# Performance work log

Measured on AMD Instinct MI355X. Metric: run time of the kernel, lower is better.

The kernel has to match this reference:

```python
import jax, jax.numpy as jnp
import numpy as np

U, H, R, N = 128, 5120, 160, 32  # users, d_inner, dt_rank, d_state(padded)


def setup_inputs() -> dict:
    key = jax.random.key(0)
    ks = jax.random.split(key, 8)
    s_in = 1.0 / np.sqrt(H)
    s_r = 1.0 / np.sqrt(R)
    x = jax.random.normal(ks[0], (1, 1, U, H), dtype=jnp.float32)
    h_prev = jnp.zeros((U, H, N), dtype=jnp.float32)
    W_dt_low = jax.random.normal(ks[1], (H, R), dtype=jnp.float32) * s_in
    W_dt = jax.random.normal(ks[2], (R, H), dtype=jnp.float32) * s_r
    b_dt = jax.random.normal(ks[3], (H,), dtype=jnp.float32) * 0.1
    W_B = jax.random.normal(ks[4], (H, N), dtype=jnp.float32) * s_in
    W_C = jax.random.normal(ks[5], (H, N), dtype=jnp.float32) * s_in
    # A = -exp(A_log): strictly negative, as in Mamba preprocessing
    A = -jnp.exp(jax.random.normal(ks[6], (H, N), dtype=jnp.float32) * 0.5)
    D = jax.random.normal(ks[7], (H,), dtype=jnp.float32)
    return {"x": x, "h_prev": h_prev, "W_dt_low": W_dt_low, "W_dt": W_dt,
            "b_dt": b_dt, "W_B": W_B, "W_C": W_C, "A": A, "D": D}


def reference(x, h_prev, W_dt_low, W_dt, b_dt, W_B, W_C, A, D):
    xf = x[0, 0]                                        # (U, H)
    # delta: low-rank projection then dt_proj + bias, softplus (beta=1, thresh=20)
    z = (xf @ W_dt_low) @ W_dt + b_dt                    # (U, H)
    delta = jnp.where(z > 20.0, z, jax.nn.softplus(z))   # (U, H)
    B = xf @ W_B                                         # (U, N)
    C = xf @ W_C                                         # (U, N)
    # discretized recurrence: h' = exp(delta*A)*h + delta*B*x
    abar = jnp.exp(delta[:, :, None] * A[None])          # (U, H, N)
    h_new = abar * h_prev + delta[:, :, None] * B[:, None, :] * xf[:, :, None]
    y = jnp.einsum('uhn,un->uh', h_new, C)               # (U, H)
    out = xf * D[None, :] + y                            # (U, H)
    return out[None, None]                               # (1, 1, U, H)
```

## Files before the change

### kernel.cpp

```cpp
#include <hip/hip_runtime.h>

#define UU 128
#define HH 5120
#define RR 160
#define NS 32

__global__ __launch_bounds__(320) void k1_dtlow(const float* __restrict__ x,
                                                const float* __restrict__ Wdl,
                                                float* __restrict__ dtlP) {
    const int ut = blockIdx.x >> 4;
    const int hc = blockIdx.x & 15;
    const int u0 = ut * 8;
    const int h0 = hc * 320;
    const int t  = threadIdx.x;
    __shared__ __attribute__((aligned(16))) float xs[320 * 8];
    #pragma unroll
    for (int i = 0; i < 8; ++i)
        xs[t * 8 + i] = x[(u0 + i) * HH + h0 + t];
    __syncthreads();
    const int r    = t % 160;
    const int half = t / 160;
    float a0 = 0.f, a1 = 0.f, a2 = 0.f, a3 = 0.f;
    const float* wp = Wdl + (size_t)h0 * RR + r;
    #pragma unroll 4
    for (int hh = 0; hh < 320; ++hh) {
        float w = wp[hh * RR];
        float4 xv = *(const float4*)&xs[hh * 8 + half * 4];
        a0 += xv.x * w; a1 += xv.y * w; a2 += xv.z * w; a3 += xv.w * w;
    }
    float* o = dtlP + hc * (UU * RR) + (u0 + half * 4) * RR + r;
    o[0] = a0; o[RR] = a1; o[2 * RR] = a2; o[3 * RR] = a3;
}

__global__ __launch_bounds__(256) void k2b_bc(const float* __restrict__ x,
                                              const float* __restrict__ WB,
                                              const float* __restrict__ WC,
                                              float* __restrict__ bcP) {
    const int ut = blockIdx.x >> 3;
    const int hc = blockIdx.x & 7;
    const int u0 = ut * 8;
    const int h0 = hc * 640;
    const int t  = threadIdx.x;
    __shared__ __attribute__((aligned(16))) float xs[640 * 8];
    for (int i = t; i < 640 * 8; i += 256) {
        int hh = i % 640, ul = i / 640;
        xs[hh * 8 + ul] = x[(u0 + ul) * HH + h0 + hh];
    }
    __syncthreads();
    const int col = t & 63, n = col & 31, mat = (col >> 5) & 1, hq = t >> 6;
    const float* W = (mat ? WC : WB) + (size_t)(h0 + hq * 160) * NS + n;
    float acc[8] = {0.f, 0.f, 0.f, 0.f, 0.f, 0.f, 0.f, 0.f};
    #pragma unroll 4
    for (int hh = 0; hh < 160; ++hh) {
        float w = W[hh * NS];
        const float* xp = &xs[(hq * 160 + hh) * 8];
        float4 a = *(const float4*)xp;
        float4 b = *(const float4*)(xp + 4);
        acc[0] += a.x * w; acc[1] += a.y * w; acc[2] += a.z * w; acc[3] += a.w * w;
        acc[4] += b.x * w; acc[5] += b.y * w; acc[6] += b.z * w; acc[7] += b.w * w;
    }
    __syncthreads();
    #pragma unroll
    for (int ul = 0; ul < 8; ++ul) xs[t * 8 + ul] = acc[ul];
    __syncthreads();
    if (hq == 0) {
        #pragma unroll
        for (int ul = 0; ul < 8; ++ul) {
            float s = xs[t * 8 + ul] + xs[(t + 64) * 8 + ul]
                    + xs[(t + 128) * 8 + ul] + xs[(t + 192) * 8 + ul];
            bcP[hc * (UU * 64) + (u0 + ul) * 64 + col] = s;
        }
    }
}

__global__ __launch_bounds__(256) void k2_delta(const float* __restrict__ dtlP,
                                                const float* __restrict__ Wdt,
                                                const float* __restrict__ bdt,
                                                const float* __restrict__ bcP,
                                                float* __restrict__ BC,
                                                float* __restrict__ delta) {
    const int ut = blockIdx.x / 20;
    const int ht = blockIdx.x % 20;
    const int u0 = ut * 8, h0 = ht * 256, t = threadIdx.x;
    __shared__ __attribute__((aligned(16))) float dtl[RR * 8];
    for (int i = t; i < RR * 8; i += 256) {
        int r = i % RR, ul = i / RR;
        float s = 0.f;
        #pragma unroll
        for (int hc = 0; hc < 16; ++hc)
            s += dtlP[hc * (UU * RR) + (u0 + ul) * RR + r];
        dtl[r * 8 + ul] = s;
    }
    if (ht == 0) {
        for (int i = t; i < 512; i += 256) {
            int ul = i >> 6, col = i & 63;
            float s = 0.f;
            #pragma unroll
            for (int hc = 0; hc < 8; ++hc)
                s += bcP[hc * (UU * 64) + (u0 + ul) * 64 + col];
            BC[(u0 + ul) * 64 + col] = s;
        }
    }
    __syncthreads();
    const int h = h0 + t;
    float acc[8] = {0.f, 0.f, 0.f, 0.f, 0.f, 0.f, 0.f, 0.f};
    #pragma unroll 4
    for (int r = 0; r < RR; ++r) {
        float w = Wdt[(size_t)r * HH + h];
        float4 a = *(const float4*)&dtl[r * 8];
        float4 b = *(const float4*)&dtl[r * 8 + 4];
        acc[0] += a.x * w; acc[1] += a.y * w; acc[2] += a.z * w; acc[3] += a.w * w;
        acc[4] += b.x * w; acc[5] += b.y * w; acc[6] += b.z * w; acc[7] += b.w * w;
    }
    const float bv = bdt[h];
    #pragma unroll
    for (int ul = 0; ul < 8; ++ul) {
        float z = acc[ul] + bv;
        float d = (z > 20.f) ? z : __logf(1.f + __expf(z));
        delta[(size_t)(u0 + ul) * HH + h] = d;
    }
}

__global__ __launch_bounds__(256) void k3_main(const float* __restrict__ x,
                                               const float* __restrict__ hprev,
                                               const float* __restrict__ A,
                                               const float* __restrict__ Dp,
                                               const float* __restrict__ BC,
                                               const float* __restrict__ delta,
                                               float* __restrict__ out) {
    const int u  = blockIdx.x / 160;
    const int ht = blockIdx.x % 160;
    const int t  = threadIdx.x;
    __shared__ __attribute__((aligned(16))) float bc[64];
    if (t < 64) bc[t] = BC[u * 64 + t];
    __syncthreads();
    const int g = t >> 3;
    const int l = t & 7;
    const int h = ht * 32 + g;
    const float d  = delta[(size_t)u * HH + h];
    const float xv = x[(size_t)u * HH + h];
    const float4 a4 = *(const float4*)&A[(size_t)h * NS + l * 4];
    const float4 hp = *(const float4*)&hprev[((size_t)u * HH + h) * NS + l * 4];
    const float4 b4 = *(const float4*)&bc[l * 4];
    const float4 c4 = *(const float4*)&bc[32 + l * 4];
    const float dx = d * xv;
    float4 hn;
    hn.x = __expf(d * a4.x) * hp.x + dx * b4.x;
    hn.y = __expf(d * a4.y) * hp.y + dx * b4.y;
    hn.z = __expf(d * a4.z) * hp.z + dx * b4.z;
    hn.w = __expf(d * a4.w) * hp.w + dx * b4.w;
    float y = hn.x * c4.x + hn.y * c4.y + hn.z * c4.z + hn.w * c4.w;
    y += __shfl_xor(y, 1);
    y += __shfl_xor(y, 2);
    y += __shfl_xor(y, 4);
    if (l == 0) out[(size_t)u * HH + h] = xv * Dp[h] + y;
}

extern "C" void kernel_launch(void* const* d_in, const int* in_sizes, int n_in,
                              void* d_out, int out_size, void* d_ws, size_t ws_size,
                              hipStream_t stream) {
    const float* x     = (const float*)d_in[0];
    const float* hprev = (const float*)d_in[1];
    const float* Wdl   = (const float*)d_in[2];
    const float* Wdt   = (const float*)d_in[3];
    const float* bdt   = (const float*)d_in[4];
    const float* WB    = (const float*)d_in[5];
    const float* WC    = (const float*)d_in[6];
    const float* A     = (const float*)d_in[7];
    const float* Dp    = (const float*)d_in[8];
    float* out = (float*)d_out;
    float* ws  = (float*)d_ws;

    float* dtlP  = ws;
    float* bcP   = ws + 327680;
    float* BC    = ws + 393216;
    float* delta = ws + 401408;

    k1_dtlow<<<256, 320, 0, stream>>>(x, Wdl, dtlP);
    k2b_bc  <<<128, 256, 0, stream>>>(x, WB, WC, bcP);
    k2_delta<<<320, 256, 0, stream>>>(dtlP, Wdt, bdt, bcP, BC, delta);
    k3_main <<<20480, 256, 0, stream>>>(x, hprev, A, Dp, BC, delta, out);
}
```

Baseline: 227.0 us.

## Fuse dt-low and B/C projections into one kernel; one thread per channel in main

Merges the low-rank dt projection and the B/C projections into a single kernel with 32 h-chunks, and transposes the partial-sum layout to [col][u] so results can be written as float4. The delta kernel now reduces over 32 partials instead of 16 and 8. The main kernel switches from 8 lanes per channel with shuffle reduction to one thread per channel looping over all 32 states, cutting the block count from 20480 to 2560. Risks include uncoalesced per-thread 128-byte hprev reads in the main kernel, 32 idle threads per block in the projection kernel, and more partial sums to reduce.

```diff
diff --git a/kernel.cpp b/kernel.cpp
--- a/kernel.cpp
+++ b/kernel.cpp
@@ -5,75 +5,56 @@
 #define RR 160
 #define NS 32
 
-__global__ __launch_bounds__(320) void k1_dtlow(const float* __restrict__ x,
-                                                const float* __restrict__ Wdl,
-                                                float* __restrict__ dtlP) {
-    const int ut = blockIdx.x >> 4;
-    const int hc = blockIdx.x & 15;
+__global__ __launch_bounds__(256) void ka_proj(const float* __restrict__ x,
+                                               const float* __restrict__ Wdl,
+                                               const float* __restrict__ WB,
+                                               const float* __restrict__ WC,
+                                               float* __restrict__ dtlP,
+                                               float* __restrict__ bcP) {
+    const int ut = blockIdx.x >> 5;
+    const int hc = blockIdx.x & 31;
     const int u0 = ut * 8;
-    const int h0 = hc * 320;
+    const int h0 = hc * 160;
     const int t  = threadIdx.x;
-    __shared__ __attribute__((aligned(16))) float xs[320 * 8];
+    __shared__ __attribute__((aligned(16))) float xs[160 * 8];
     #pragma unroll
-    for (int i = 0; i < 8; ++i)
-        xs[t * 8 + i] = x[(u0 + i) * HH + h0 + t];
-    __syncthreads();
-    const int r    = t % 160;
-    const int half = t / 160;
-    float a0 = 0.f, a1 = 0.f, a2 = 0.f, a3 = 0.f;
-    const float* wp = Wdl + (size_t)h0 * RR + r;
-    #pragma unroll 4
-    for (int hh = 0; hh < 320; ++hh) {
-        float w = wp[hh * RR];
-        float4 xv = *(const float4*)&xs[hh * 8 + half * 4];
-        a0 += xv.x * w; a1 += xv.y * w; a2 += xv.z * w; a3 += xv.w * w;
-    }
-    float* o = dtlP + hc * (UU * RR) + (u0 + half * 4) * RR + r;
-    o[0] = a0; o[RR] = a1; o[2 * RR] = a2; o[3 * RR] = a3;
-}
-
-__global__ __launch_bounds__(256) void k2b_bc(const float* __restrict__ x,
-                                              const float* __restrict__ WB,
-                                              const float* __restrict__ WC,
-                                              float* __restrict__ bcP) {
-    const int ut = blockIdx.x >> 3;
-    const int hc = blockIdx.x & 7;
-    const int u0 = ut * 8;
-    const int h0 = hc * 640;
-    const int t  = threadIdx.x;
-    __shared__ __attribute__((aligned(16))) float xs[640 * 8];
-    for (int i = t; i < 640 * 8; i += 256) {
-        int hh = i % 640, ul = i / 640;
+    for (int k = 0; k < 5; ++k) {
+        int i  = t + k * 256;
+        int ul = i / 160, hh = i % 160;
         xs[hh * 8 + ul] = x[(u0 + ul) * HH + h0 + hh];
     }
     __syncthreads();
-    const int col = t & 63, n = col & 31, mat = (col >> 5) & 1, hq = t >> 6;
-    const float* W = (mat ? WC : WB) + (size_t)(h0 + hq * 160) * NS + n;
-    float acc[8] = {0.f, 0.f, 0.f, 0.f, 0.f, 0.f, 0.f, 0.f};
+    const int c = t;
+    const float* wp;
+    int stride;
+    float* outp = nullptr;
+    if (c < 160) {
+        wp = Wdl + (size_t)h0 * RR + c;          stride = RR;
+        outp = dtlP + hc * (RR * UU) + c * UU + u0;
+    } else if (c < 224) {
+        int col = c - 160;
+        wp = ((col < 32) ? WB : WC) + (size_t)h0 * NS + (col & 31);
+        stride = NS;
+        outp = bcP + hc * (64 * UU) + col * UU + u0;
+    } else {
+        wp = Wdl; stride = 0;
+    }
+    float a[8] = {0.f, 0.f, 0.f, 0.f, 0.f, 0.f, 0.f, 0.f};
     #pragma unroll 4
     for (int hh = 0; hh < 160; ++hh) {
-        float w = W[hh * NS];
-        const float* xp = &xs[(hq * 160 + hh) * 8];
-        float4 a = *(const float4*)xp;
-        float4 b = *(const float4*)(xp + 4);
-        acc[0] += a.x * w; acc[1] += a.y * w; acc[2] += a.z * w; acc[3] += a.w * w;
-        acc[4] += b.x * w; acc[5] += b.y * w; acc[6] += b.z * w; acc[7] += b.w * w;
+        float w = wp[hh * stride];
+        float4 x0 = *(const float4*)&xs[hh * 8];
+        float4 x1 = *(const float4*)&xs[hh * 8 + 4];
+        a[0] += x0.x * w; a[1] += x0.y * w; a[2] += x0.z * w; a[3] += x0.w * w;
+        a[4] += x1.x * w; a[5] += x1.y * w; a[6] += x1.z * w; a[7] += x1.w * w;
     }
-    __syncthreads();
-    #pragma unroll
-    for (int ul = 0; ul < 8; ++ul) xs[t * 8 + ul] = acc[ul];
-    __syncthreads();
-    if (hq == 0) {
-        #pragma unroll
-        for (int ul = 0; ul < 8; ++ul) {
-            float s = xs[t * 8 + ul] + xs[(t + 64) * 8 + ul]
-                    + xs[(t + 128) * 8 + ul] + xs[(t + 192) * 8 + ul];
-            bcP[hc * (UU * 64) + (u0 + ul) * 64 + col] = s;
-        }
+    if (outp) {
+        *(float4*)&outp[0] = make_float4(a[0], a[1], a[2], a[3]);
+        *(float4*)&outp[4] = make_float4(a[4], a[5], a[6], a[7]);
     }
 }
 
-__global__ __launch_bounds__(256) void k2_delta(const float* __restrict__ dtlP,
+__global__ __launch_bounds__(256) void kb_delta(const float* __restrict__ dtlP,
                                                 const float* __restrict__ Wdt,
                                                 const float* __restrict__ bdt,
                                                 const float* __restrict__ bcP,
@@ -83,21 +64,25 @@
     const int ht = blockIdx.x % 20;
     const int u0 = ut * 8, h0 = ht * 256, t = threadIdx.x;
     __shared__ __attribute__((aligned(16))) float dtl[RR * 8];
-    for (int i = t; i < RR * 8; i += 256) {
-        int r = i % RR, ul = i / RR;
+    #pragma unroll
+    for (int k = 0; k < 5; ++k) {
+        int i = t + k * 256;
+        int r = i >> 3, ul = i & 7;
         float s = 0.f;
         #pragma unroll
-        for (int hc = 0; hc < 16; ++hc)
-            s += dtlP[hc * (UU * RR) + (u0 + ul) * RR + r];
-        dtl[r * 8 + ul] = s;
+        for (int hc = 0; hc < 32; ++hc)
+            s += dtlP[hc * (RR * UU) + r * UU + u0 + ul];
+        dtl[i] = s;
     }
     if (ht == 0) {
-        for (int i = t; i < 512; i += 256) {
+        #pragma unroll
+        for (int k = 0; k < 2; ++k) {
+            int i = t + k * 256;
             int ul = i >> 6, col = i & 63;
             float s = 0.f;
             #pragma unroll
-            for (int hc = 0; hc < 8; ++hc)
-                s += bcP[hc * (UU * 64) + (u0 + ul) * 64 + col];
+            for (int hc = 0; hc < 32; ++hc)
+                s += bcP[hc * (64 * UU) + col * UU + u0 + ul];
             BC[(u0 + ul) * 64 + col] = s;
         }
     }
@@ -121,39 +106,39 @@
     }
 }
 
-__global__ __launch_bounds__(256) void k3_main(const float* __restrict__ x,
+__global__ __launch_bounds__(256) void kc_main(const float* __restrict__ x,
                                                const float* __restrict__ hprev,
                                                const float* __restrict__ A,
                                                const float* __restrict__ Dp,
                                                const float* __restrict__ BC,
                                                const float* __restrict__ delta,
                                                float* __restrict__ out) {
-    const int u  = blockIdx.x / 160;
-    const int ht = blockIdx.x % 160;
+    const int u  = blockIdx.x / 20;
+    const int ht = blockIdx.x % 20;
     const int t  = threadIdx.x;
     __shared__ __attribute__((aligned(16))) float bc[64];
     if (t < 64) bc[t] = BC[u * 64 + t];
     __syncthreads();
-    const int g = t >> 3;
-    const int l = t & 7;
-    const int h = ht * 32 + g;
+    const int h = ht * 256 + t;
     const float d  = delta[(size_t)u * HH + h];
     const float xv = x[(size_t)u * HH + h];
-    const float4 a4 = *(const float4*)&A[(size_t)h * NS + l * 4];
-    const float4 hp = *(const float4*)&hprev[((size_t)u * HH + h) * NS + l * 4];
-    const float4 b4 = *(const float4*)&bc[l * 4];
-    const float4 c4 = *(const float4*)&bc[32 + l * 4];
     const float dx = d * xv;
-    float4 hn;
-    hn.x = __expf(d * a4.x) * hp.x + dx * b4.x;
-    hn.y = __expf(d * a4.y) * hp.y + dx * b4.y;
-    hn.z = __expf(d * a4.z) * hp.z + dx * b4.z;
-    hn.w = __expf(d * a4.w) * hp.w + dx * b4.w;
-    float y = hn.x * c4.x + hn.y * c4.y + hn.z * c4.z + hn.w * c4.w;
-    y += __shfl_xor(y, 1);
-    y += __shfl_xor(y, 2);
-    y += __shfl_xor(y, 4);
-    if (l == 0) out[(size_t)u * HH + h] = xv * Dp[h] + y;
+    const float4* hp = (const float4*)&hprev[((size_t)u * HH + h) * NS];
+    const float4* ap = (const float4*)&A[(size_t)h * NS];
+    float y = 0.f;
+    #pragma unroll
+    for (int j = 0; j < 8; ++j) {
+        float4 a4 = ap[j];
+        float4 h4 = hp[j];
+        float4 b4 = *(const float4*)&bc[j * 4];
+        float4 c4 = *(const float4*)&bc[32 + j * 4];
+        float n0 = __expf(d * a4.x) * h4.x + dx * b4.x;
+        float n1 = __expf(d * a4.y) * h4.y + dx * b4.y;
+        float n2 = __expf(d * a4.z) * h4.z + dx * b4.z;
+        float n3 = __expf(d * a4.w) * h4.w + dx * b4.w;
+        y += n0 * c4.x + n1 * c4.y + n2 * c4.z + n3 * c4.w;
+    }
+    out[(size_t)u * HH + h] = xv * Dp[h] + y;
 }
 
 extern "C" void kernel_launch(void* const* d_in, const int* in_sizes, int n_in,
@@ -172,12 +157,11 @@
     float* ws  = (float*)d_ws;
 
     float* dtlP  = ws;
-    float* bcP   = ws + 327680;
-    float* BC    = ws + 393216;
-    float* delta = ws + 401408;
+    float* bcP   = ws + 655360;
+    float* BC    = ws + 917504;
+    float* delta = ws + 925696;
 
-    k1_dtlow<<<256, 320, 0, stream>>>(x, Wdl, dtlP);
-    k2b_bc  <<<128, 256, 0, stream>>>(x, WB, WC, bcP);
-    k2_delta<<<320, 256, 0, stream>>>(dtlP, Wdt, bdt, bcP, BC, delta);
-    k3_main <<<20480, 256, 0, stream>>>(x, hprev, A, Dp, BC, delta, out);
+    ka_proj <<<512,  256, 0, stream>>>(x, Wdl, WB, WC, dtlP, bcP);
+    kb_delta<<<320,  256, 0, stream>>>(dtlP, Wdt, bdt, bcP, BC, delta);
+    kc_main <<<2560, 256, 0, stream>>>(x, hprev, A, Dp, BC, delta, out);
 }
```

Result: faster. 214.9 us (-5.3%).
